# Kernel optimization log

Measured on AMD Instinct MI355X. Metric: run time of the kernel, lower is better.

## Reference

```python
import jax, jax.numpy as jnp
import numpy as np

N = 50000
E = 800000
IN_DIM = 18
HID = 32
HEADS = 4
NEG_SLOPE = 0.2
LN_EPS = 1e-5


def setup_inputs() -> dict:
    key = jax.random.key(0)
    ks = jax.random.split(key, 16)
    def rn(k, shape, scale=0.1):
        return jax.random.normal(k, shape, dtype=jnp.float32) * scale
    inp = {}
    inp['x'] = jax.random.normal(ks[0], (N, IN_DIM), dtype=jnp.float32)
    inp['edge_index'] = jax.random.randint(ks[1], (2, E), 0, N)
    # layer dims: (in, heads, out, concat)
    dims = [(IN_DIM, HEADS, HID, True), (HID * HEADS, HEADS, HID, True), (HID * HEADS, 1, HID, False)]
    i = 2
    for l, (din, h, dout, concat) in enumerate(dims):
        inp[f'Wl{l}'] = rn(ks[i], (din, h * dout)); i += 1
        inp[f'bl{l}'] = jnp.zeros((h * dout,), jnp.float32)
        inp[f'Wr{l}'] = rn(ks[i], (din, h * dout)); i += 1
        inp[f'br{l}'] = jnp.zeros((h * dout,), jnp.float32)
        inp[f'att{l}'] = rn(ks[i], (h, dout)); i += 1
        ldim = h * dout if concat else dout
        inp[f'bo{l}'] = jnp.zeros((ldim,), jnp.float32)
        inp[f'g{l}'] = jnp.ones((ldim,), jnp.float32)
        inp[f'be{l}'] = jnp.zeros((ldim,), jnp.float32)
    inp['cW1'] = rn(ks[i], (HID, HID // 2)); i += 1
    inp['cb1'] = jnp.zeros((HID // 2,), jnp.float32)
    inp['cW2'] = rn(ks[i], (HID // 2, 1)); i += 1
    inp['cb2'] = jnp.zeros((1,), jnp.float32)
    return inp


def _layer_norm(h, g, b):
    mu = h.mean(-1, keepdims=True)
    var = h.var(-1, keepdims=True)
    return (h - mu) * jax.lax.rsqrt(var + LN_EPS) * g + b


def _gatv2(x, src, dst, Wl, bl, Wr, br, att, bo, heads, dout, concat):
    # PyG GATv2Conv (eval mode): x_j via lin_l (source), x_i via lin_r (target)
    n = x.shape[0]
    xl = (x @ Wl + bl).reshape(n, heads, dout)
    xr = (x @ Wr + br).reshape(n, heads, dout)
    e = jax.nn.leaky_relu(xl[src] + xr[dst], NEG_SLOPE)          # [E, H, D]
    logits = jnp.einsum('ehd,hd->eh', e, att)                    # [E, H]
    m = jax.ops.segment_max(logits, dst, num_segments=n)         # scatter-softmax over dst
    a = jnp.exp(logits - m[dst])
    denom = jax.ops.segment_sum(a, dst, num_segments=n)
    alpha = a / denom[dst]                                       # [E, H]
    out = jax.ops.segment_sum(xl[src] * alpha[:, :, None], dst, num_segments=n)
    out = out.reshape(n, heads * dout) if concat else out.mean(axis=1)
    return out + bo


def _forward(x, src, dst, params):
    h_in = x
    for (Wl, bl, Wr, br, att, bo, g, be, heads, dout, concat) in params[:-1]:
        pass
    layers = params
    for i, (Wl, bl, Wr, br, att, bo, g, be, heads, dout, concat) in enumerate(layers):
        h = _gatv2(h_in, src, dst, Wl, bl, Wr, br, att, bo, heads, dout, concat)
        h = jax.nn.elu(_layer_norm(h, g, be))
        if i > 0 and h.shape == h_in.shape:
            h = h + h_in
        h_in = h
    return h_in


def reference(x, edge_index, Wl0, bl0, Wr0, br0, att0, bo0, g0, be0,
              Wl1, bl1, Wr1, br1, att1, bo1, g1, be1,
              Wl2, bl2, Wr2, br2, att2, bo2, g2, be2,
              cW1, cb1, cW2, cb2):
    n = x.shape[0]
    loop = jnp.arange(n, dtype=edge_index.dtype)  # add_self_loops=True
    src = jnp.concatenate([edge_index[0], loop])
    dst = jnp.concatenate([edge_index[1], loop])
    params = [
        (Wl0, bl0, Wr0, br0, att0, bo0, g0, be0, HEADS, HID, True),
        (Wl1, bl1, Wr1, br1, att1, bo1, g1, be1, HEADS, HID, True),
        (Wl2, bl2, Wr2, br2, att2, bo2, g2, be2, 1, HID, False),
    ]
    h = _forward(x, src, dst, params)
    h = jax.nn.elu(h @ cW1 + cb1)
    out = (h @ cW2 + cb2).squeeze(-1)
    return out
```

## Files before the change

kernel.cpp:

```cpp
#include <hip/hip_runtime.h>
#include <math.h>

#define N_NODES 50000
#define N_EDGES 800000
#define ET (N_EDGES + N_NODES)


__global__ void k_init_deg(int* deg, int n) {
    int i = blockIdx.x * blockDim.x + threadIdx.x;
    if (i < n) deg[i] = 1;
}

__global__ void k_count(const int* __restrict__ dst, int* __restrict__ deg, int e) {
    int i = blockIdx.x * blockDim.x + threadIdx.x;
    if (i < e) atomicAdd(&deg[dst[i]], 1);
}

__global__ void k_scan(const int* __restrict__ deg, int* __restrict__ rowptr,
                       int* __restrict__ cursor, int n) {
    __shared__ int wsum[16];
    __shared__ int carry_sh;
    int t = threadIdx.x;
    int wid = t >> 6, lane = t & 63;
    if (t == 0) carry_sh = 0;
    __syncthreads();
    for (int base = 0; base < n; base += 1024) {
        int i = base + t;
        int v = (i < n) ? deg[i] : 0;
        int x = v;
#pragma unroll
        for (int off = 1; off < 64; off <<= 1) {
            int u = __shfl_up(x, off, 64);
            if (lane >= off) x += u;
        }
        if (lane == 63) wsum[wid] = x;
        __syncthreads();
        if (wid == 0) {
            int wv = (lane < 16) ? wsum[lane] : 0;
            int y = wv;
#pragma unroll
            for (int off = 1; off < 16; off <<= 1) {
                int u = __shfl_up(y, off, 64);
                if (lane >= off) y += u;
            }
            if (lane < 16) wsum[lane] = y - wv;
        }
        __syncthreads();
        int carry = carry_sh;
        int excl = carry + wsum[wid] + x - v;
        if (i < n) { rowptr[i] = excl; cursor[i] = excl; }
        __syncthreads();
        if (t == 1023) carry_sh = excl + v;
        __syncthreads();
    }
    if (t == 0) rowptr[n] = carry_sh;
}

__global__ void k_fill(const int* __restrict__ src, const int* __restrict__ dst,
                       int* __restrict__ cursor, int* __restrict__ csr_src) {
    int i = blockIdx.x * blockDim.x + threadIdx.x;
    if (i < N_EDGES) {
        int d = dst[i];
        int pos = atomicAdd(&cursor[d], 1);
        csr_src[pos] = src[i];
    } else if (i < ET) {
        int node = i - N_EDGES;
        int pos = atomicAdd(&cursor[node], 1);
        csr_src[pos] = node;
    }
}


__global__ void k_zero256(int* hist) { hist[threadIdx.x] = 0; }

__global__ void k_hist(const int* __restrict__ deg, int* __restrict__ hist, int n) {
    __shared__ int lh[256];
    lh[threadIdx.x] = 0;
    __syncthreads();
    for (int i = blockIdx.x * 256 + threadIdx.x; i < n; i += gridDim.x * 256) {
        int b = deg[i]; b = (b > 255) ? 255 : b;
        atomicAdd(&lh[b], 1);
    }
    __syncthreads();
    if (lh[threadIdx.x]) atomicAdd(&hist[threadIdx.x], lh[threadIdx.x]);
}

__global__ void k_binstart(const int* __restrict__ hist, int* __restrict__ bincur) {
    __shared__ int sh[256];
    int t = threadIdx.x;
    int v = hist[t];
    sh[t] = v;
    __syncthreads();
    for (int off = 1; off < 256; off <<= 1) {
        int u = (t >= off) ? sh[t - off] : 0;
        __syncthreads();
        sh[t] += u;
        __syncthreads();
    }
    bincur[t] = sh[t] - v;
}

__global__ void k_scatter(const int* __restrict__ deg, int* __restrict__ bincur,
                          int* __restrict__ order, int n) {
    __shared__ int lcount[256];
    __shared__ int lbase[256];
    int t = threadIdx.x;
    lcount[t] = 0;
    __syncthreads();
    int i = blockIdx.x * 256 + t;
    int b = 0, rank = 0;
    bool valid = (i < n);
    if (valid) {
        b = deg[i]; b = (b > 255) ? 255 : b;
        rank = atomicAdd(&lcount[b], 1);
    }
    __syncthreads();
    if (lcount[t] > 0) lbase[t] = atomicAdd(&bincur[t], lcount[t]);
    __syncthreads();
    if (valid) order[lbase[b] + rank] = i;
}


template<int K, int BK, int HD, int BN, int TM, int TN>
__launch_bounds__(256, 4)
__global__ void k_gemm_t(const float* __restrict__ x,
                         const float* __restrict__ Wl, const float* __restrict__ bl,
                         const float* __restrict__ Wr, const float* __restrict__ br,
                         float* __restrict__ xl, float* __restrict__ xr, int n) {
    constexpr int BM = 128;
    constexpr int CT_PER = HD / BN;
    __shared__ float xs[BK][BM + 4];
    __shared__ float ws[BK][BN];
    int m0 = blockIdx.x * BM;
    int ct = blockIdx.y;
    const float* W  = (ct < CT_PER) ? Wl : Wr;
    const float* bv = (ct < CT_PER) ? bl : br;
    float* o        = (ct < CT_PER) ? xl : xr;
    int colBase = (ct % CT_PER) * BN;
    int t = threadIdx.x;
    int tr = t >> 4, tc = t & 15;
    float acc[TM][TN];
#pragma unroll
    for (int j = 0; j < TN; j++) {
        float b0 = bv[colBase + tc * TN + j];
#pragma unroll
        for (int i = 0; i < TM; i++) acc[i][j] = b0;
    }
    for (int k0 = 0; k0 < K; k0 += BK) {
        if constexpr ((BK % 4) == 0) {
            constexpr int NFL4 = BM * BK / 4;
            for (int idx = t; idx < NFL4; idx += 256) {
                int r  = idx % BM;
                int c0 = idx / BM;
                float4 v = {0.f, 0.f, 0.f, 0.f};
                int row = m0 + r;
                if (row < n) v = *(const float4*)&x[(size_t)row * K + k0 + c0 * 4];
                xs[c0 * 4 + 0][r] = v.x;
                xs[c0 * 4 + 1][r] = v.y;
                xs[c0 * 4 + 2][r] = v.z;
                xs[c0 * 4 + 3][r] = v.w;
            }
        } else {
            for (int idx = t; idx < BM * BK; idx += 256) {
                int r = idx % BM;
                int c = idx / BM;
                float v = 0.f;
                int row = m0 + r;
                if (row < n) v = x[(size_t)row * K + k0 + c];
                xs[c][r] = v;
            }
        }
        for (int idx = t; idx < BK * BN; idx += 256) {
            int r = idx / BN, c = idx % BN;
            ws[r][c] = W[(size_t)(k0 + r) * HD + colBase + c];
        }
        __syncthreads();
#pragma unroll 2
        for (int k = 0; k < BK; k++) {
            float a[TM], b[TN];
#pragma unroll
            for (int q = 0; q < TM; q += 4)
                *(float4*)&a[q] = *(const float4*)&xs[k][tr * TM + q];
            if constexpr (TN == 8) {
                *(float4*)&b[0] = *(const float4*)&ws[k][tc * TN];
                *(float4*)&b[4] = *(const float4*)&ws[k][tc * TN + 4];
            } else if constexpr (TN == 4) {
                *(float4*)&b[0] = *(const float4*)&ws[k][tc * TN];
            } else {
                *(float2*)&b[0] = *(const float2*)&ws[k][tc * TN];
            }
#pragma unroll
            for (int i = 0; i < TM; i++)
#pragma unroll
                for (int j = 0; j < TN; j++)
                    acc[i][j] = fmaf(a[i], b[j], acc[i][j]);
        }
        __syncthreads();
    }
#pragma unroll
    for (int i = 0; i < TM; i++) {
        int r = m0 + tr * TM + i;
        if (r < n) {
            if constexpr ((TN % 4) == 0) {
#pragma unroll
                for (int j = 0; j < TN; j += 4)
                    *(float4*)&o[(size_t)r * HD + colBase + tc * TN + j] = *(float4*)&acc[i][j];
            } else {
                *(float2*)&o[(size_t)r * HD + colBase + tc * TN] = *(float2*)&acc[i][0];
            }
        }
    }
}


template<int HD, int D, bool RES, bool CLS>
__global__ void k_gather_ln(const float* __restrict__ xl, const float* __restrict__ xr,
                            const float* __restrict__ att,
                            const int* __restrict__ rowptr, const int* __restrict__ csr_src,
                            const int* __restrict__ order,
                            const float* __restrict__ bo, const float* __restrict__ g,
                            const float* __restrict__ be, const float* res,
                            float* outh,
                            const float* cW1, const float* cb1,
                            const float* cW2, const float* cb2,
                            float* out, int n) {
    constexpr int VEC = 8;
    constexpr int L = HD / VEC;
    constexpr int NPW = 64 / L;
    constexpr int G = D / VEC;
    __shared__ float w1s[CLS ? 512 : 1];
    __shared__ float b1s[CLS ? 16 : 1];
    __shared__ float w2s[CLS ? 16 : 1];
    __shared__ float b2s[1];
    if (CLS) {
        int t = threadIdx.x;
        for (int i = t; i < 512; i += blockDim.x) w1s[i] = cW1[i];
        if (t < 16) { b1s[t] = cb1[t]; w2s[t] = cW2[t]; }
        if (t == 0) b2s[0] = cb2[0];
        __syncthreads();
    }
    int tid = blockIdx.x * blockDim.x + threadIdx.x;
    int wave = tid >> 6;
    int lane = tid & 63;
    int slot = wave * NPW + lane / L;
    if (slot >= n) return;
    int node = order[slot];
    int sub = lane % L;
    int f = sub * VEC;

    float xrv[8], attv[8], acc[8];
    {
        const float4* xrp = (const float4*)(xr + (size_t)node * HD + f);
        float4 a0 = xrp[0], a1 = xrp[1];
        xrv[0]=a0.x; xrv[1]=a0.y; xrv[2]=a0.z; xrv[3]=a0.w;
        xrv[4]=a1.x; xrv[5]=a1.y; xrv[6]=a1.z; xrv[7]=a1.w;
        const float4* ap = (const float4*)(att + f);
        float4 t0 = ap[0], t1 = ap[1];
        attv[0]=t0.x; attv[1]=t0.y; attv[2]=t0.z; attv[3]=t0.w;
        attv[4]=t1.x; attv[5]=t1.y; attv[6]=t1.z; attv[7]=t1.w;
#pragma unroll
        for (int i = 0; i < 8; i++) acc[i] = 0.f;
    }
    int e0 = rowptr[node];
    int deg = rowptr[node + 1] - e0;
    float denom = 0.f;
    int npairs = deg >> 1;

    float4 ua0, ua1, ub0, ub1;
    if (npairs > 0) {
        int sa = csr_src[e0];
        int sb = csr_src[e0 + 1];
        const float4* pa = (const float4*)(xl + (size_t)sa * HD + f);
        const float4* pb = (const float4*)(xl + (size_t)sb * HD + f);
        ua0 = pa[0]; ua1 = pa[1]; ub0 = pb[0]; ub1 = pb[1];
    }
    for (int p = 0; p < npairs; p++) {
        float4 ca0 = ua0, ca1 = ua1, cb0 = ub0, cb1 = ub1;
        if (p + 1 < npairs) {
            int na = csr_src[e0 + 2 * p + 2];
            int nb = csr_src[e0 + 2 * p + 3];
            const float4* pa = (const float4*)(xl + (size_t)na * HD + f);
            const float4* pb = (const float4*)(xl + (size_t)nb * HD + f);
            ua0 = pa[0]; ua1 = pa[1]; ub0 = pb[0]; ub1 = pb[1];
        }
        float xa[8] = {ca0.x, ca0.y, ca0.z, ca0.w, ca1.x, ca1.y, ca1.z, ca1.w};
        float xb[8] = {cb0.x, cb0.y, cb0.z, cb0.w, cb1.x, cb1.y, cb1.z, cb1.w};
        float pA = 0.f, pB = 0.f;
#pragma unroll
        for (int i = 0; i < 8; i++) {
            float ea = xa[i] + xrv[i];
            float eb = xb[i] + xrv[i];
            ea = (ea > 0.f) ? ea : 0.2f * ea;
            eb = (eb > 0.f) ? eb : 0.2f * eb;
            pA = fmaf(ea, attv[i], pA);
            pB = fmaf(eb, attv[i], pB);
        }
#pragma unroll
        for (int msk = G / 2; msk >= 1; msk >>= 1) {
            pA += __shfl_xor(pA, msk, 64);
            pB += __shfl_xor(pB, msk, 64);
        }
        float wA = __expf(pA);
        float wB = __expf(pB);
        denom += wA + wB;
#pragma unroll
        for (int i = 0; i < 8; i++) {
            acc[i] = fmaf(wA, xa[i], acc[i]);
            acc[i] = fmaf(wB, xb[i], acc[i]);
        }
    }
    if (deg & 1) {
        int s = csr_src[e0 + deg - 1];
        const float4* xp = (const float4*)(xl + (size_t)s * HD + f);
        float4 c0 = xp[0], c1 = xp[1];
        float xa[8] = {c0.x, c0.y, c0.z, c0.w, c1.x, c1.y, c1.z, c1.w};
        float pA = 0.f;
#pragma unroll
        for (int i = 0; i < 8; i++) {
            float ea = xa[i] + xrv[i];
            ea = (ea > 0.f) ? ea : 0.2f * ea;
            pA = fmaf(ea, attv[i], pA);
        }
#pragma unroll
        for (int msk = G / 2; msk >= 1; msk >>= 1) pA += __shfl_xor(pA, msk, 64);
        float wA = __expf(pA);
        denom += wA;
#pragma unroll
        for (int i = 0; i < 8; i++) acc[i] = fmaf(wA, xa[i], acc[i]);
    }
    float inv = 1.f / denom;
    float v[8];
    float s1 = 0.f;
#pragma unroll
    for (int i = 0; i < 8; i++) {
        v[i] = acc[i] * inv + bo[f + i];
        s1 += v[i];
    }
#pragma unroll
    for (int msk = L / 2; msk >= 1; msk >>= 1) s1 += __shfl_xor(s1, msk, 64);
    float mu = s1 * (1.f / HD);
    float q = 0.f;
#pragma unroll
    for (int i = 0; i < 8; i++) { float d = v[i] - mu; q += d * d; }
#pragma unroll
    for (int msk = L / 2; msk >= 1; msk >>= 1) q += __shfl_xor(q, msk, 64);
    float rstd = rsqrtf(q * (1.f / HD) + 1e-5f);
    float y[8];
#pragma unroll
    for (int i = 0; i < 8; i++) {
        float t = (v[i] - mu) * rstd * g[f + i] + be[f + i];
        t = (t > 0.f) ? t : expm1f(t);
        if (RES) t += res[(size_t)node * HD + f + i];
        y[i] = t;
    }
    if constexpr (!CLS) {
        float4 o0 = {y[0], y[1], y[2], y[3]};
        float4 o1 = {y[4], y[5], y[6], y[7]};
        float4* op = (float4*)(outh + (size_t)node * HD + f);
        op[0] = o0; op[1] = o1;
    } else {
        float pj[16];
#pragma unroll
        for (int j = 0; j < 16; j++) pj[j] = 0.f;
#pragma unroll
        for (int k = 0; k < 8; k++) {
#pragma unroll
            for (int j = 0; j < 16; j++)
                pj[j] = fmaf(y[k], w1s[(f + k) * 16 + j], pj[j]);
        }
#pragma unroll
        for (int j = 0; j < 16; j++) {
            pj[j] += __shfl_xor(pj[j], 1, 64);
            pj[j] += __shfl_xor(pj[j], 2, 64);
        }
        float o = b2s[0];
#pragma unroll
        for (int j = 0; j < 16; j++) {
            float a2 = pj[j] + b1s[j];
            a2 = (a2 > 0.f) ? a2 : expm1f(a2);
            o = fmaf(a2, w2s[j], o);
        }
        if (sub == 0) out[node] = o;
    }
}


extern "C" void kernel_launch(void* const* d_in, const int* in_sizes, int n_in,
                              void* d_out, int out_size, void* d_ws, size_t ws_size,
                              hipStream_t stream) {
    (void)in_sizes; (void)n_in; (void)out_size; (void)ws_size;
    const float* x  = (const float*)d_in[0];
    const int*   ei = (const int*)d_in[1];
    const int* src = ei;
    const int* dst = ei + N_EDGES;

    const float* Wl0 = (const float*)d_in[2];
    const float* bl0 = (const float*)d_in[3];
    const float* Wr0 = (const float*)d_in[4];
    const float* br0 = (const float*)d_in[5];
    const float* att0= (const float*)d_in[6];
    const float* bo0 = (const float*)d_in[7];
    const float* g0  = (const float*)d_in[8];
    const float* be0 = (const float*)d_in[9];
    const float* Wl1 = (const float*)d_in[10];
    const float* bl1 = (const float*)d_in[11];
    const float* Wr1 = (const float*)d_in[12];
    const float* br1 = (const float*)d_in[13];
    const float* att1= (const float*)d_in[14];
    const float* bo1 = (const float*)d_in[15];
    const float* g1  = (const float*)d_in[16];
    const float* be1 = (const float*)d_in[17];
    const float* Wl2 = (const float*)d_in[18];
    const float* bl2 = (const float*)d_in[19];
    const float* Wr2 = (const float*)d_in[20];
    const float* br2 = (const float*)d_in[21];
    const float* att2= (const float*)d_in[22];
    const float* bo2 = (const float*)d_in[23];
    const float* g2  = (const float*)d_in[24];
    const float* be2 = (const float*)d_in[25];
    const float* cW1 = (const float*)d_in[26];
    const float* cb1 = (const float*)d_in[27];
    const float* cW2 = (const float*)d_in[28];
    const float* cb2 = (const float*)d_in[29];

    char* ws = (char*)d_ws;
    float* xl = (float*)ws; ws += (size_t)N_NODES * 128 * 4;
    float* xr = (float*)ws; ws += (size_t)N_NODES * 128 * 4;
    float* h0 = (float*)ws; ws += (size_t)N_NODES * 128 * 4;
    float* h1 = (float*)ws; ws += (size_t)N_NODES * 128 * 4;
    int* rowptr  = (int*)ws; ws += (size_t)(N_NODES + 1) * 4;
    int* cursor  = (int*)ws; ws += (size_t)N_NODES * 4;
    int* deg     = (int*)ws; ws += (size_t)N_NODES * 4;
    int* csr_src = (int*)ws; ws += (size_t)ET * 4;
    int* hist    = (int*)ws; ws += 256 * 4;
    int* bincur  = (int*)ws; ws += 256 * 4;
    int* order   = (int*)ws; ws += (size_t)N_NODES * 4;

    k_init_deg<<<(N_NODES + 255) / 256, 256, 0, stream>>>(deg, N_NODES);
    k_count<<<(N_EDGES + 255) / 256, 256, 0, stream>>>(dst, deg, N_EDGES);
    k_scan<<<1, 1024, 0, stream>>>(deg, rowptr, cursor, N_NODES);
    k_fill<<<(ET + 255) / 256, 256, 0, stream>>>(src, dst, cursor, csr_src);
    k_zero256<<<1, 256, 0, stream>>>(hist);
    k_hist<<<64, 256, 0, stream>>>(deg, hist, N_NODES);
    k_binstart<<<1, 256, 0, stream>>>(hist, bincur);
    k_scatter<<<(N_NODES + 255) / 256, 256, 0, stream>>>(deg, bincur, order, N_NODES);

    const int gx128 = (N_NODES + 127) / 128;
    const int gridG128 = (N_NODES + 15) / 16;
    const int gridG32  = (N_NODES + 63) / 64;

    k_gemm_t<18, 18, 128, 128, 8, 8><<<dim3(gx128, 2), 256, 0, stream>>>(
        x, Wl0, bl0, Wr0, br0, xl, xr, N_NODES);
    k_gather_ln<128, 32, false, false><<<gridG128, 256, 0, stream>>>(
        xl, xr, att0, rowptr, csr_src, order, bo0, g0, be0, nullptr, h0,
        nullptr, nullptr, nullptr, nullptr, nullptr, N_NODES);

    k_gemm_t<128, 32, 128, 128, 8, 8><<<dim3(gx128, 2), 256, 0, stream>>>(
        h0, Wl1, bl1, Wr1, br1, xl, xr, N_NODES);
    k_gather_ln<128, 32, true, false><<<gridG128, 256, 0, stream>>>(
        xl, xr, att1, rowptr, csr_src, order, bo1, g1, be1, h0, h1,
        nullptr, nullptr, nullptr, nullptr, nullptr, N_NODES);

    k_gemm_t<128, 32, 32, 32, 8, 2><<<dim3(gx128, 2), 256, 0, stream>>>(
        h1, Wl2, bl2, Wr2, br2, xl, xr, N_NODES);
    k_gather_ln<32, 32, false, true><<<gridG32, 256, 0, stream>>>(
        xl, xr, att2, rowptr, csr_src, order, bo2, g2, be2, nullptr, nullptr,
        cW1, cb1, cW2, cb2, (float*)d_out, N_NODES);
}
```

Baseline: 557.4 us.

## Store projected features as fp16 head-major and split gather from LayerNorm

The GEMM now writes xl/xr in half precision in a head-major layout ([head][node][32]), halving the bytes moved by the random per-edge gathers. The gather is rewritten as a per-head kernel, with blocks interleaved across heads so each head's 3.2MB slice can stay cache-resident. LayerNorm, ELU, residual and the classifier move into a separate kernel that reads an fp32 intermediate buffer. This adds an extra write and read of an N×128 fp32 array and an extra launch per layer, and fp16 storage reduces the precision of the attention inputs.

```diff
diff --git a/kernel.cpp b/kernel.cpp
--- a/kernel.cpp
+++ b/kernel.cpp
@@ -4,6 +4,8 @@
 #define N_NODES 50000
 #define N_EDGES 800000
 #define ET (N_EDGES + N_NODES)
+
+typedef _Float16 f16;
 
 
 __global__ void k_init_deg(int* deg, int n) {
@@ -126,7 +128,7 @@
 __global__ void k_gemm_t(const float* __restrict__ x,
                          const float* __restrict__ Wl, const float* __restrict__ bl,
                          const float* __restrict__ Wr, const float* __restrict__ br,
-                         float* __restrict__ xl, float* __restrict__ xr, int n) {
+                         f16* __restrict__ xlh, f16* __restrict__ xrh, int n) {
     constexpr int BM = 128;
     constexpr int CT_PER = HD / BN;
     __shared__ float xs[BK][BM + 4];
@@ -135,7 +137,7 @@
     int ct = blockIdx.y;
     const float* W  = (ct < CT_PER) ? Wl : Wr;
     const float* bv = (ct < CT_PER) ? bl : br;
-    float* o        = (ct < CT_PER) ? xl : xr;
+    f16* o          = (ct < CT_PER) ? xlh : xrh;
     int colBase = (ct % CT_PER) * BN;
     int t = threadIdx.x;
     int tr = t >> 4, tc = t & 15;
@@ -197,37 +199,145 @@
         }
         __syncthreads();
     }
+    int col0 = colBase + tc * TN;
+    int hh = col0 >> 5;
+    int cc = col0 & 31;
 #pragma unroll
     for (int i = 0; i < TM; i++) {
         int r = m0 + tr * TM + i;
         if (r < n) {
-            if constexpr ((TN % 4) == 0) {
-#pragma unroll
-                for (int j = 0; j < TN; j += 4)
-                    *(float4*)&o[(size_t)r * HD + colBase + tc * TN + j] = *(float4*)&acc[i][j];
-            } else {
-                *(float2*)&o[(size_t)r * HD + colBase + tc * TN] = *(float2*)&acc[i][0];
-            }
-        }
-    }
-}
-
-
-template<int HD, int D, bool RES, bool CLS>
-__global__ void k_gather_ln(const float* __restrict__ xl, const float* __restrict__ xr,
-                            const float* __restrict__ att,
-                            const int* __restrict__ rowptr, const int* __restrict__ csr_src,
-                            const int* __restrict__ order,
-                            const float* __restrict__ bo, const float* __restrict__ g,
-                            const float* __restrict__ be, const float* res,
-                            float* outh,
-                            const float* cW1, const float* cb1,
-                            const float* cW2, const float* cb2,
-                            float* out, int n) {
-    constexpr int VEC = 8;
-    constexpr int L = HD / VEC;
+            alignas(16) f16 hb[TN];
+#pragma unroll
+            for (int j = 0; j < TN; j++) hb[j] = (f16)acc[i][j];
+            f16* dst = o + (size_t)hh * (N_NODES * 32) + (size_t)r * 32 + cc;
+            if constexpr (TN == 8)      *(float4*)dst = *(float4*)hb;
+            else if constexpr (TN == 4) *(float2*)dst = *(float2*)hb;
+            else                        *(float*)dst  = *(float*)hb;
+        }
+    }
+}
+
+
+template<int NH>
+__global__ void k_gather_h(const f16* __restrict__ xlh, const f16* __restrict__ xrh,
+                           const float* __restrict__ att,
+                           const int* __restrict__ rowptr, const int* __restrict__ csr_src,
+                           const int* __restrict__ order,
+                           float* __restrict__ out, int n) {
+    constexpr int HD = NH * 32;
+    int bid = blockIdx.x;
+    int head, nodeblk;
+    if constexpr (NH == 4) {
+        head = (bid & 7) >> 1;
+        nodeblk = (bid >> 3) * 2 + (bid & 1);
+    } else {
+        head = 0;
+        nodeblk = bid;
+    }
+    int lane = threadIdx.x & 63;
+    int slot = nodeblk * 64 + (threadIdx.x >> 6) * 16 + (lane >> 2);
+    if (slot >= n) return;
+    int node = order[slot];
+    int sub = lane & 3;
+    const size_t hbase = (size_t)head * (N_NODES * 32);
+    const int fh = head * 32 + sub * 8;
+
+    float xrv[8], attv[8], acc[8];
+    {
+        float4 raw = *(const float4*)(xrh + hbase + (size_t)node * 32 + sub * 8);
+        const f16* hp = (const f16*)&raw;
+#pragma unroll
+        for (int i = 0; i < 8; i++) xrv[i] = (float)hp[i];
+        const float4* ap = (const float4*)(att + fh);
+        float4 t0 = ap[0], t1 = ap[1];
+        attv[0]=t0.x; attv[1]=t0.y; attv[2]=t0.z; attv[3]=t0.w;
+        attv[4]=t1.x; attv[5]=t1.y; attv[6]=t1.z; attv[7]=t1.w;
+#pragma unroll
+        for (int i = 0; i < 8; i++) acc[i] = 0.f;
+    }
+    int e0 = rowptr[node];
+    int deg = rowptr[node + 1] - e0;
+    float denom = 0.f;
+    int npairs = deg >> 1;
+
+    float4 ua, ub;
+    if (npairs > 0) {
+        int sa = csr_src[e0];
+        int sb = csr_src[e0 + 1];
+        ua = *(const float4*)(xlh + hbase + (size_t)sa * 32 + sub * 8);
+        ub = *(const float4*)(xlh + hbase + (size_t)sb * 32 + sub * 8);
+    }
+    for (int p = 0; p < npairs; p++) {
+        float4 ca = ua, cb = ub;
+        if (p + 1 < npairs) {
+            int na = csr_src[e0 + 2 * p + 2];
+            int nb = csr_src[e0 + 2 * p + 3];
+            ua = *(const float4*)(xlh + hbase + (size_t)na * 32 + sub * 8);
+            ub = *(const float4*)(xlh + hbase + (size_t)nb * 32 + sub * 8);
+        }
+        const f16* ha = (const f16*)&ca;
+        const f16* hb = (const f16*)&cb;
+        float xa[8], xb[8];
+#pragma unroll
+        for (int i = 0; i < 8; i++) { xa[i] = (float)ha[i]; xb[i] = (float)hb[i]; }
+        float pA = 0.f, pB = 0.f;
+#pragma unroll
+        for (int i = 0; i < 8; i++) {
+            float ea = xa[i] + xrv[i];
+            float eb = xb[i] + xrv[i];
+            ea = (ea > 0.f) ? ea : 0.2f * ea;
+            eb = (eb > 0.f) ? eb : 0.2f * eb;
+            pA = fmaf(ea, attv[i], pA);
+            pB = fmaf(eb, attv[i], pB);
+        }
+        pA += __shfl_xor(pA, 1, 64); pA += __shfl_xor(pA, 2, 64);
+        pB += __shfl_xor(pB, 1, 64); pB += __shfl_xor(pB, 2, 64);
+        float wA = __expf(pA);
+        float wB = __expf(pB);
+        denom += wA + wB;
+#pragma unroll
+        for (int i = 0; i < 8; i++) {
+            acc[i] = fmaf(wA, xa[i], acc[i]);
+            acc[i] = fmaf(wB, xb[i], acc[i]);
+        }
+    }
+    if (deg & 1) {
+        int s = csr_src[e0 + deg - 1];
+        float4 ca = *(const float4*)(xlh + hbase + (size_t)s * 32 + sub * 8);
+        const f16* ha = (const f16*)&ca;
+        float xa[8];
+#pragma unroll
+        for (int i = 0; i < 8; i++) xa[i] = (float)ha[i];
+        float pA = 0.f;
+#pragma unroll
+        for (int i = 0; i < 8; i++) {
+            float ea = xa[i] + xrv[i];
+            ea = (ea > 0.f) ? ea : 0.2f * ea;
+            pA = fmaf(ea, attv[i], pA);
+        }
+        pA += __shfl_xor(pA, 1, 64); pA += __shfl_xor(pA, 2, 64);
+        float wA = __expf(pA);
+        denom += wA;
+#pragma unroll
+        for (int i = 0; i < 8; i++) acc[i] = fmaf(wA, xa[i], acc[i]);
+    }
+    float inv = 1.f / denom;
+    float4 o0 = {acc[0]*inv, acc[1]*inv, acc[2]*inv, acc[3]*inv};
+    float4 o1 = {acc[4]*inv, acc[5]*inv, acc[6]*inv, acc[7]*inv};
+    float4* op = (float4*)(out + (size_t)node * HD + fh);
+    op[0] = o0; op[1] = o1;
+}
+
+
+template<int HD, bool RES, bool CLS>
+__global__ void k_ln(const float* __restrict__ in, const float* __restrict__ bo,
+                     const float* __restrict__ g, const float* __restrict__ be,
+                     const float* res, float* outh,
+                     const float* cW1, const float* cb1,
+                     const float* cW2, const float* cb2,
+                     float* out, int n) {
+    constexpr int L = HD / 8;
     constexpr int NPW = 64 / L;
-    constexpr int G = D / VEC;
     __shared__ float w1s[CLS ? 512 : 1];
     __shared__ float b1s[CLS ? 16 : 1];
     __shared__ float w2s[CLS ? 16 : 1];
@@ -242,100 +352,20 @@
     int tid = blockIdx.x * blockDim.x + threadIdx.x;
     int wave = tid >> 6;
     int lane = tid & 63;
-    int slot = wave * NPW + lane / L;
-    if (slot >= n) return;
-    int node = order[slot];
+    int node = wave * NPW + lane / L;
+    if (node >= n) return;
     int sub = lane % L;
-    int f = sub * VEC;
-
-    float xrv[8], attv[8], acc[8];
+    int f = sub * 8;
+    float v[8];
     {
-        const float4* xrp = (const float4*)(xr + (size_t)node * HD + f);
-        float4 a0 = xrp[0], a1 = xrp[1];
-        xrv[0]=a0.x; xrv[1]=a0.y; xrv[2]=a0.z; xrv[3]=a0.w;
-        xrv[4]=a1.x; xrv[5]=a1.y; xrv[6]=a1.z; xrv[7]=a1.w;
-        const float4* ap = (const float4*)(att + f);
-        float4 t0 = ap[0], t1 = ap[1];
-        attv[0]=t0.x; attv[1]=t0.y; attv[2]=t0.z; attv[3]=t0.w;
-        attv[4]=t1.x; attv[5]=t1.y; attv[6]=t1.z; attv[7]=t1.w;
-#pragma unroll
-        for (int i = 0; i < 8; i++) acc[i] = 0.f;
-    }
-    int e0 = rowptr[node];
-    int deg = rowptr[node + 1] - e0;
-    float denom = 0.f;
-    int npairs = deg >> 1;
-
-    float4 ua0, ua1, ub0, ub1;
-    if (npairs > 0) {
-        int sa = csr_src[e0];
-        int sb = csr_src[e0 + 1];
-        const float4* pa = (const float4*)(xl + (size_t)sa * HD + f);
-        const float4* pb = (const float4*)(xl + (size_t)sb * HD + f);
-        ua0 = pa[0]; ua1 = pa[1]; ub0 = pb[0]; ub1 = pb[1];
-    }
-    for (int p = 0; p < npairs; p++) {
-        float4 ca0 = ua0, ca1 = ua1, cb0 = ub0, cb1 = ub1;
-        if (p + 1 < npairs) {
-            int na = csr_src[e0 + 2 * p + 2];
-            int nb = csr_src[e0 + 2 * p + 3];
-            const float4* pa = (const float4*)(xl + (size_t)na * HD + f);
-            const float4* pb = (const float4*)(xl + (size_t)nb * HD + f);
-            ua0 = pa[0]; ua1 = pa[1]; ub0 = pb[0]; ub1 = pb[1];
-        }
-        float xa[8] = {ca0.x, ca0.y, ca0.z, ca0.w, ca1.x, ca1.y, ca1.z, ca1.w};
-        float xb[8] = {cb0.x, cb0.y, cb0.z, cb0.w, cb1.x, cb1.y, cb1.z, cb1.w};
-        float pA = 0.f, pB = 0.f;
-#pragma unroll
-        for (int i = 0; i < 8; i++) {
-            float ea = xa[i] + xrv[i];
-            float eb = xb[i] + xrv[i];
-            ea = (ea > 0.f) ? ea : 0.2f * ea;
-            eb = (eb > 0.f) ? eb : 0.2f * eb;
-            pA = fmaf(ea, attv[i], pA);
-            pB = fmaf(eb, attv[i], pB);
-        }
-#pragma unroll
-        for (int msk = G / 2; msk >= 1; msk >>= 1) {
-            pA += __shfl_xor(pA, msk, 64);
-            pB += __shfl_xor(pB, msk, 64);
-        }
-        float wA = __expf(pA);
-        float wB = __expf(pB);
-        denom += wA + wB;
-#pragma unroll
-        for (int i = 0; i < 8; i++) {
-            acc[i] = fmaf(wA, xa[i], acc[i]);
-            acc[i] = fmaf(wB, xb[i], acc[i]);
-        }
-    }
-    if (deg & 1) {
-        int s = csr_src[e0 + deg - 1];
-        const float4* xp = (const float4*)(xl + (size_t)s * HD + f);
-        float4 c0 = xp[0], c1 = xp[1];
-        float xa[8] = {c0.x, c0.y, c0.z, c0.w, c1.x, c1.y, c1.z, c1.w};
-        float pA = 0.f;
-#pragma unroll
-        for (int i = 0; i < 8; i++) {
-            float ea = xa[i] + xrv[i];
-            ea = (ea > 0.f) ? ea : 0.2f * ea;
-            pA = fmaf(ea, attv[i], pA);
-        }
-#pragma unroll
-        for (int msk = G / 2; msk >= 1; msk >>= 1) pA += __shfl_xor(pA, msk, 64);
-        float wA = __expf(pA);
-        denom += wA;
-#pragma unroll
-        for (int i = 0; i < 8; i++) acc[i] = fmaf(wA, xa[i], acc[i]);
-    }
-    float inv = 1.f / denom;
-    float v[8];
+        const float4* ip = (const float4*)(in + (size_t)node * HD + f);
+        float4 a0 = ip[0], a1 = ip[1];
+        v[0]=a0.x; v[1]=a0.y; v[2]=a0.z; v[3]=a0.w;
+        v[4]=a1.x; v[5]=a1.y; v[6]=a1.z; v[7]=a1.w;
+    }
     float s1 = 0.f;
 #pragma unroll
-    for (int i = 0; i < 8; i++) {
-        v[i] = acc[i] * inv + bo[f + i];
-        s1 += v[i];
-    }
+    for (int i = 0; i < 8; i++) { v[i] += bo[f + i]; s1 += v[i]; }
 #pragma unroll
     for (int msk = L / 2; msk >= 1; msk >>= 1) s1 += __shfl_xor(s1, msk, 64);
     float mu = s1 * (1.f / HD);
@@ -424,10 +454,11 @@
     const float* cb2 = (const float*)d_in[29];
 
     char* ws = (char*)d_ws;
-    float* xl = (float*)ws; ws += (size_t)N_NODES * 128 * 4;
-    float* xr = (float*)ws; ws += (size_t)N_NODES * 128 * 4;
-    float* h0 = (float*)ws; ws += (size_t)N_NODES * 128 * 4;
-    float* h1 = (float*)ws; ws += (size_t)N_NODES * 128 * 4;
+    f16* xlh   = (f16*)ws;   ws += (size_t)N_NODES * 128 * 2;
+    f16* xrh   = (f16*)ws;   ws += (size_t)N_NODES * 128 * 2;
+    float* gout = (float*)ws; ws += (size_t)N_NODES * 128 * 4;
+    float* h0  = (float*)ws; ws += (size_t)N_NODES * 128 * 4;
+    float* h1  = (float*)ws; ws += (size_t)N_NODES * 128 * 4;
     int* rowptr  = (int*)ws; ws += (size_t)(N_NODES + 1) * 4;
     int* cursor  = (int*)ws; ws += (size_t)N_NODES * 4;
     int* deg     = (int*)ws; ws += (size_t)N_NODES * 4;
@@ -446,24 +477,29 @@
     k_scatter<<<(N_NODES + 255) / 256, 256, 0, stream>>>(deg, bincur, order, N_NODES);
 
     const int gx128 = (N_NODES + 127) / 128;
-    const int gridG128 = (N_NODES + 15) / 16;
-    const int gridG32  = (N_NODES + 63) / 64;
+    const int nodeblks = (N_NODES + 63) / 64;
+    const int gridGH4 = ((nodeblks + 1) / 2) * 8;
+    const int gridLN128 = (N_NODES + 15) / 16;
+    const int gridLN32  = nodeblks;
 
     k_gemm_t<18, 18, 128, 128, 8, 8><<<dim3(gx128, 2), 256, 0, stream>>>(
-        x, Wl0, bl0, Wr0, br0, xl, xr, N_NODES);
-    k_gather_ln<128, 32, false, false><<<gridG128, 256, 0, stream>>>(
-        xl, xr, att0, rowptr, csr_src, order, bo0, g0, be0, nullptr, h0,
-        nullptr, nullptr, nullptr, nullptr, nullptr, N_NODES);
+        x, Wl0, bl0, Wr0, br0, xlh, xrh, N_NODES);
+    k_gather_h<4><<<gridGH4, 256, 0, stream>>>(
+        xlh, xrh, att0, rowptr, csr_src, order, gout, N_NODES);
+    k_ln<128, false, false><<<gridLN128, 256, 0, stream>>>(
+        gout, bo0, g0, be0, nullptr, h0, nullptr, nullptr, nullptr, nullptr, nullptr, N_NODES);
 
     k_gemm_t<128, 32, 128, 128, 8, 8><<<dim3(gx128, 2), 256, 0, stream>>>(
-        h0, Wl1, bl1, Wr1, br1, xl, xr, N_NODES);
-    k_gather_ln<128, 32, true, false><<<gridG128, 256, 0, stream>>>(
-        xl, xr, att1, rowptr, csr_src, order, bo1, g1, be1, h0, h1,
-        nullptr, nullptr, nullptr, nullptr, nullptr, N_NODES);
+        h0, Wl1, bl1, Wr1, br1, xlh, xrh, N_NODES);
+    k_gather_h<4><<<gridGH4, 256, 0, stream>>>(
+        xlh, xrh, att1, rowptr, csr_src, order, gout, N_NODES);
+    k_ln<128, true, false><<<gridLN128, 256, 0, stream>>>(
+        gout, bo1, g1, be1, h0, h1, nullptr, nullptr, nullptr, nullptr, nullptr, N_NODES);
 
     k_gemm_t<128, 32, 32, 32, 8, 2><<<dim3(gx128, 2), 256, 0, stream>>>(
-        h1, Wl2, bl2, Wr2, br2, xl, xr, N_NODES);
-    k_gather_ln<32, 32, false, true><<<gridG32, 256, 0, stream>>>(
-        xl, xr, att2, rowptr, csr_src, order, bo2, g2, be2, nullptr, nullptr,
-        cW1, cb1, cW2, cb2, (float*)d_out, N_NODES);
-}
+        h1, Wl2, bl2, Wr2, br2, xlh, xrh, N_NODES);
+    k_gather_h<1><<<nodeblks, 256, 0, stream>>>(
+        xlh, xrh, att2, rowptr, csr_src, order, gout, N_NODES);
+    k_ln<32, false, true><<<gridLN32, 256, 0, stream>>>(
+        gout, bo2, g2, be2, nullptr, nullptr, cW1, cb1, cW2, cb2, (float*)d_out, N_NODES);
+}
```

Measured after the change: 547.0 us. Within noise of the previous version (-1.9%).
